# Performance work log

Hardware: AMD Instinct MI355X
Metric: run time of the kernel (lower is better)

Reference implementation:

```python
import jax, jax.numpy as jnp
import numpy as np

N_TOKEN = 32000
N_LAYER = 6
N_HEAD = 16
D_MODEL = 1024
D_HEAD = 64
D_INNER = 4096
QLEN = 512
MEM_LEN = 512
BSZ = 8
HD = N_HEAD * D_HEAD
SCALE = 1.0 / float(np.sqrt(D_HEAD))
NEG = -1e30


def _layer_norm(x, g, b, eps=1e-5):
    mu = jnp.mean(x, axis=-1, keepdims=True)
    var = jnp.var(x, axis=-1, keepdims=True)
    return (x - mu) * jax.lax.rsqrt(var + eps) * g + b


def _rel_shift(x):
    # x: [qlen, klen, bsz, n_head] -- TXL relative-position shift
    q, k, b, n = x.shape
    zp = jnp.zeros((q, 1, b, n), x.dtype)
    xp = jnp.concatenate([zp, x], axis=1).reshape(k + 1, q, b, n)
    return xp[1:].reshape(q, k, b, n)


def setup_inputs():
    key = jax.random.key(0)
    ks = jax.random.split(key, 12)
    s = 0.02
    rn = lambda k, *sh: jax.random.normal(k, sh, jnp.float32) * s
    z = lambda *sh: jnp.zeros(sh, jnp.float32)
    o = lambda *sh: jnp.ones(sh, jnp.float32)
    return {
        "data": jax.random.randint(ks[0], (QLEN, BSZ), 0, N_TOKEN),
        "target": jax.random.randint(ks[1], (QLEN, BSZ), 0, N_TOKEN),
        "memory": jax.random.normal(ks[2], (N_LAYER, MEM_LEN, BSZ, D_MODEL), jnp.float32),
        "emb_W": rn(ks[3], N_TOKEN, D_MODEL),  # tied input embedding / softmax head
        "r_w_bias": rn(ks[4], N_HEAD, D_HEAD),
        "r_r_bias": rn(ks[5], N_HEAD, D_HEAD),
        "Wq": rn(ks[6], N_LAYER, D_MODEL, HD),
        "Wkv": rn(ks[7], N_LAYER, D_MODEL, 2 * HD),
        "Wr": rn(ks[8], N_LAYER, D_MODEL, HD),
        "Wo": rn(ks[9], N_LAYER, HD, D_MODEL),
        "W1": rn(ks[10], N_LAYER, D_MODEL, D_INNER),
        "b1": z(N_LAYER, D_INNER),
        "W2": rn(ks[11], N_LAYER, D_INNER, D_MODEL),
        "b2": z(N_LAYER, D_MODEL),
        "ln1_g": o(N_LAYER, D_MODEL),
        "ln1_b": z(N_LAYER, D_MODEL),
        "ln2_g": o(N_LAYER, D_MODEL),
        "ln2_b": z(N_LAYER, D_MODEL),
    }


def _model(data, target, memory, emb_W, r_w_bias, r_r_bias, Wq, Wkv, Wr, Wo,
           W1, b1, W2, b2, ln1_g, ln1_b, ln2_g, ln2_b):
    qlen, bsz = data.shape
    mem = jax.lax.stop_gradient(memory)  # TXL detaches memories
    mlen = mem.shape[1]
    klen = mlen + qlen

    word_emb = emb_W[data]  # [q, b, d]

    # sinusoidal relative positions klen-1 .. 0
    pos_seq = jnp.arange(klen - 1, -1, -1, dtype=word_emb.dtype)
    inv_freq = 1.0 / (10000.0 ** (jnp.arange(0, D_MODEL, 2, dtype=word_emb.dtype) / D_MODEL))
    sin_inp = pos_seq[:, None] * inv_freq[None, :]
    pos = jnp.concatenate([jnp.sin(sin_inp), jnp.cos(sin_inp)], axis=-1)  # [klen, d]

    # causal mask with memory: query i can attend keys j <= i + mlen
    mask = jnp.arange(klen)[None, :] > (jnp.arange(qlen)[:, None] + mlen)  # [q, k]

    core = word_emb
    hids = [core]
    for i in range(N_LAYER):
        x_mem = jnp.concatenate([mem[i], core], axis=0)  # [klen, b, d]
        q = (core @ Wq[i]).reshape(qlen, bsz, N_HEAD, D_HEAD)
        kv = x_mem @ Wkv[i]
        k, v = jnp.split(kv, 2, axis=-1)
        k = k.reshape(klen, bsz, N_HEAD, D_HEAD)
        v = v.reshape(klen, bsz, N_HEAD, D_HEAD)
        r_k = (pos @ Wr[i]).reshape(klen, N_HEAD, D_HEAD)

        AC = jnp.einsum('ibnd,jbnd->ijbn', q + r_w_bias, k)
        BD = _rel_shift(jnp.einsum('ibnd,jnd->ijbn', q + r_r_bias, r_k))
        score = (AC + BD) * SCALE
        score = jnp.where(mask[:, :, None, None], NEG, score)
        prob = jax.nn.softmax(score, axis=1)
        vec = jnp.einsum('ijbn,jbnd->ibnd', prob, v).reshape(qlen, bsz, HD)
        attn_out = vec @ Wo[i]
        core = _layer_norm(core + attn_out, ln1_g[i], ln1_b[i])
        ff = jax.nn.relu(core @ W1[i] + b1[i]) @ W2[i] + b2[i]
        core = _layer_norm(core + ff, ln2_g[i], ln2_b[i])
        hids.append(core)

    # adaptive softmax with cutoffs=[] == full tied softmax
    logits = core @ emb_W.T  # [q, b, V]
    logp = jax.nn.log_softmax(logits, axis=-1)
    loss = -jnp.take_along_axis(logp, target[..., None], axis=-1)[..., 0]  # [q, b]

    new_mems = jnp.stack([
        jnp.concatenate([mem[i], hids[i]], axis=0)[-MEM_LEN:] for i in range(N_LAYER)
    ])
    new_mems = jax.lax.stop_gradient(new_mems)
    return loss, new_mems


def reference(data, target, memory, emb_W, r_w_bias, r_r_bias, Wq, Wkv, Wr, Wo,
              W1, b1, W2, b2, ln1_g, ln1_b, ln2_g, ln2_b):
    return _model(data, target, memory, emb_W, r_w_bias, r_r_bias, Wq, Wkv, Wr, Wo,
                  W1, b1, W2, b2, ln1_g, ln1_b, ln2_g, ln2_b)
```

## Files before the change

### kernel.cpp

```cpp
#include <hip/hip_runtime.h>
#include <hip/hip_bf16.h>
#include <math.h>

#define QLEN   512
#define MLEN   512
#define KLEN   1024
#define BSZ    8
#define NH     16
#define DH     64
#define DM     1024
#define DI     4096
#define NTOK   32000
#define NROW   4096
#define XROW   8192
#define VTILES 500

typedef __hip_bfloat16 bf16;
typedef __attribute__((ext_vector_type(8))) short bf16x8;
typedef __attribute__((ext_vector_type(4))) float f32x4;

__device__ __forceinline__ unsigned short f2b(float x) {
    union { float f; unsigned u; } a; a.f = x;
    unsigned r = a.u + 0x7fffu + ((a.u >> 16) & 1u);
    return (unsigned short)(r >> 16);
}
__device__ __forceinline__ float b2f(unsigned short h) {
    union { unsigned u; float f; } a; a.u = ((unsigned)h) << 16;
    return a.f;
}

__device__ __forceinline__ void gload_lds16(const void* g, void* l) {
    __builtin_amdgcn_global_load_lds(
        (const __attribute__((address_space(1))) unsigned int*)g,
        (__attribute__((address_space(3))) unsigned int*)l, 16, 0, 0);
}

__global__ __launch_bounds__(256) void posb_kernel(unsigned short* __restrict__ posb) {
    int j = blockIdx.x;
    int t = threadIdx.x;
    float p = (float)(1023 - j);
    #pragma unroll
    for (int u = 0; u < 4; u++) {
        int dcol = t + u * 256;
        int k = dcol & 511;
        float invf = expf(-((float)k) * (1.0f / 512.0f) * 9.210340371976184f);
        float a = p * invf;
        posb[j * DM + dcol] = f2b((dcol < 512) ? sinf(a) : cosf(a));
    }
}

__global__ __launch_bounds__(256) void gather_emb(const int* __restrict__ data,
                                                  const float* __restrict__ emb,
                                                  float* __restrict__ out,
                                                  unsigned short* __restrict__ outb) {
    int row = blockIdx.x;
    int t = threadIdx.x;
    int tok = data[row];
    float4 v = ((const float4*)(emb + (size_t)tok * DM))[t];
    ((float4*)(out + (size_t)row * DM))[t] = v;
    ushort4 o;
    o.x = f2b(v.x); o.y = f2b(v.y); o.z = f2b(v.z); o.w = f2b(v.w);
    ((ushort4*)(outb + (size_t)row * DM))[t] = o;
}

__global__ __launch_bounds__(256) void cast_bf16(const float* __restrict__ src,
                                                 unsigned short* __restrict__ dst, int n4) {
    int i = blockIdx.x * 256 + threadIdx.x;
    if (i < n4) {
        float4 v = ((const float4*)src)[i];
        ushort4 o;
        o.x = f2b(v.x); o.y = f2b(v.y); o.z = f2b(v.z); o.w = f2b(v.w);
        ((ushort4*)dst)[i] = o;
    }
}

__global__ __launch_bounds__(256) void castT_kernel(const float* __restrict__ src,
                                                    unsigned short* __restrict__ dst,
                                                    int K, int N) {
    __shared__ float T[32][33];
    int t = threadIdx.x;
    int k0 = blockIdx.y * 32, n0 = blockIdx.x * 32;
    int r = t >> 3, c4 = (t & 7) * 4;
    float4 v = *(const float4*)(src + (size_t)(k0 + r) * N + n0 + c4);
    T[r][c4 + 0] = v.x; T[r][c4 + 1] = v.y; T[r][c4 + 2] = v.z; T[r][c4 + 3] = v.w;
    __syncthreads();
    ushort4 o;
    o.x = f2b(T[c4 + 0][r]); o.y = f2b(T[c4 + 1][r]);
    o.z = f2b(T[c4 + 2][r]); o.w = f2b(T[c4 + 3][r]);
    *(ushort4*)(dst + (size_t)(n0 + r) * K + k0 + c4) = o;
}

template <bool BIAS, bool RELU, bool OUTBF16, int SPLITK = 1>
__global__ __launch_bounds__(256) void gemm_bt(const unsigned short* __restrict__ A,
                                               const unsigned short* __restrict__ B,
                                               const float* __restrict__ bias,
                                               void* __restrict__ Cout,
                                               int M, int N, int K) {
    __shared__ unsigned short As[128 * 32];
    __shared__ unsigned short Bs[128 * 32];
    int t = threadIdx.x;
    int wave = t >> 6, lane = t & 63;
    int bm = blockIdx.y * 128, bn = blockIdx.x * 128;
    int wm = (wave >> 1) * 64, wn = (wave & 1) * 64;
    int quad = lane >> 4, l16 = lane & 15;

    f32x4 acc[4][4] = {};

    int srow = wave * 32 + (lane >> 2);
    int scol = (lane & 3) * 8;
    const unsigned short* Ag = A + (size_t)(bm + srow) * K + scol;
    const unsigned short* Bg = B + (size_t)(bn + srow) * K + scol;
    unsigned short* Al0 = As + (wave * 32) * 32;
    unsigned short* Al1 = As + (wave * 32 + 16) * 32;
    unsigned short* Bl0 = Bs + (wave * 32) * 32;
    unsigned short* Bl1 = Bs + (wave * 32 + 16) * 32;

    int kchunk = K / SPLITK;
    int k0 = (SPLITK > 1) ? blockIdx.z * kchunk : 0;
    for (int kt = k0; kt < k0 + kchunk; kt += 32) {
        gload_lds16(Ag + kt, Al0);
        gload_lds16(Ag + kt + (size_t)16 * K, Al1);
        gload_lds16(Bg + kt, Bl0);
        gload_lds16(Bg + kt + (size_t)16 * K, Bl1);
        __syncthreads();
        bf16x8 af[4], bfr[4];
        #pragma unroll
        for (int mi = 0; mi < 4; mi++)
            af[mi] = *(const bf16x8*)&As[(wm + mi * 16 + l16) * 32 + quad * 8];
        #pragma unroll
        for (int ni = 0; ni < 4; ni++)
            bfr[ni] = *(const bf16x8*)&Bs[(wn + ni * 16 + l16) * 32 + quad * 8];
        #pragma unroll
        for (int mi = 0; mi < 4; mi++)
            #pragma unroll
            for (int ni = 0; ni < 4; ni++)
                acc[mi][ni] = __builtin_amdgcn_mfma_f32_16x16x32_bf16(
                    af[mi], bfr[ni], acc[mi][ni], 0, 0, 0);
        __syncthreads();
    }

    float* Cf = (float*)Cout + ((SPLITK > 1) ? (size_t)blockIdx.z * M * N : (size_t)0);
    #pragma unroll
    for (int mi = 0; mi < 4; mi++) {
        #pragma unroll
        for (int ni = 0; ni < 4; ni++) {
            int c = bn + wn + ni * 16 + l16;
            float bv = BIAS ? bias[c] : 0.0f;
            #pragma unroll
            for (int reg = 0; reg < 4; reg++) {
                int r = bm + wm + mi * 16 + quad * 4 + reg;
                float x = acc[mi][ni][reg];
                if (BIAS) x += bv;
                if (RELU) x = fmaxf(x, 0.0f);
                if (OUTBF16) ((unsigned short*)Cout)[(size_t)r * N + c] = f2b(x);
                else         Cf[(size_t)r * N + c] = x;
            }
        }
    }
}

__global__ __launch_bounds__(256) void kqv_gemm(const unsigned short* __restrict__ A,
                                                const unsigned short* __restrict__ B,
                                                const float* __restrict__ rwb,
                                                const float* __restrict__ rrb,
                                                unsigned short* __restrict__ qw,
                                                unsigned short* __restrict__ qr,
                                                unsigned short* __restrict__ Kh,
                                                unsigned short* __restrict__ Vth) {
    int cls = blockIdx.x >> 3;
    if (cls == 0 && blockIdx.y < 32) return;
    __shared__ unsigned short As[128 * 32];
    __shared__ unsigned short Bs[128 * 32];
    const int K = 1024;
    int t = threadIdx.x;
    int wave = t >> 6, lane = t & 63;
    int bm = blockIdx.y * 128, bn = blockIdx.x * 128;
    int wm = (wave >> 1) * 64, wn = (wave & 1) * 64;
    int quad = lane >> 4, l16 = lane & 15;

    f32x4 acc[4][4] = {};

    int srow = wave * 32 + (lane >> 2);
    int scol = (lane & 3) * 8;
    const unsigned short* Ag = A + (size_t)(bm + srow) * K + scol;
    const unsigned short* Bg = B + (size_t)(bn + srow) * K + scol;
    unsigned short* Al0 = As + (wave * 32) * 32;
    unsigned short* Al1 = As + (wave * 32 + 16) * 32;
    unsigned short* Bl0 = Bs + (wave * 32) * 32;
    unsigned short* Bl1 = Bs + (wave * 32 + 16) * 32;

    for (int kt = 0; kt < K; kt += 32) {
        gload_lds16(Ag + kt, Al0);
        gload_lds16(Ag + kt + (size_t)16 * K, Al1);
        gload_lds16(Bg + kt, Bl0);
        gload_lds16(Bg + kt + (size_t)16 * K, Bl1);
        __syncthreads();
        bf16x8 af[4], bfr[4];
        #pragma unroll
        for (int mi = 0; mi < 4; mi++)
            af[mi] = *(const bf16x8*)&As[(wm + mi * 16 + l16) * 32 + quad * 8];
        #pragma unroll
        for (int ni = 0; ni < 4; ni++)
            bfr[ni] = *(const bf16x8*)&Bs[(wn + ni * 16 + l16) * 32 + quad * 8];
        #pragma unroll
        for (int mi = 0; mi < 4; mi++)
            #pragma unroll
            for (int ni = 0; ni < 4; ni++)
                acc[mi][ni] = __builtin_amdgcn_mfma_f32_16x16x32_bf16(
                    af[mi], bfr[ni], acc[mi][ni], 0, 0, 0);
        __syncthreads();
    }

    if (cls == 0) {
        #pragma unroll
        for (int ni = 0; ni < 4; ni++) {
            int c = bn + wn + ni * 16 + l16;
            float wv = rwb[c], rv = rrb[c];
            #pragma unroll
            for (int mi = 0; mi < 4; mi++) {
                #pragma unroll
                for (int reg = 0; reg < 4; reg++) {
                    int r = bm + wm + mi * 16 + quad * 4 + reg;
                    int row = r - 4096;
                    int i = row >> 3;
                    float x = acc[mi][ni][reg];
                    qr[(size_t)row * DM + c] = f2b(x + rv);
                    qw[(size_t)row * DM + (c & ~63) + ((c & 63) ^ ((i & 7) << 3))] = f2b(x + wv);
                }
            }
        }
    } else if (cls == 1) {
        #pragma unroll
        for (int ni = 0; ni < 4; ni++) {
            int cc = bn + wn + ni * 16 + l16 - 1024;
            int d = cc & 63, hb = cc >> 6;
            #pragma unroll
            for (int mi = 0; mi < 4; mi++) {
                #pragma unroll
                for (int reg = 0; reg < 4; reg++) {
                    int r = bm + wm + mi * 16 + quad * 4 + reg;
                    int j = r >> 3, nb = hb * 8 + (r & 7);
                    Kh[(size_t)nb * 65536 + (size_t)j * 64 + (d ^ ((j & 7) << 3))] =
                        f2b(acc[mi][ni][reg]);
                }
            }
        }
    } else {
        #pragma unroll
        for (int ni = 0; ni < 4; ni++) {
            int cc = bn + wn + ni * 16 + l16 - 2048;
            int d = cc & 63, hb = cc >> 6;
            #pragma unroll
            for (int mi = 0; mi < 4; mi++) {
                #pragma unroll
                for (int reg = 0; reg < 4; reg++) {
                    int r = bm + wm + mi * 16 + quad * 4 + reg;
                    int j = r >> 3, nb = hb * 8 + (r & 7);
                    Vth[(size_t)nb * 65536 + (size_t)d * 1024
                        + (j & ~127) + ((j & 127) ^ ((d & 7) << 3))] =
                        f2b(acc[mi][ni][reg]);
                }
            }
        }
    }
}

__global__ __launch_bounds__(256) void lse_gemm_mfma(const unsigned short* __restrict__ A,
                                                     const unsigned short* __restrict__ B,
                                                     float* __restrict__ pmax,
                                                     float* __restrict__ psum) {
    __shared__ unsigned short As[128 * 32];
    __shared__ unsigned short Bs[128 * 32];
    int t = threadIdx.x;
    int wave = t >> 6, lane = t & 63;
    int bm = blockIdx.x * 128, bn = blockIdx.y * 128;
    int wm = (wave >> 1) * 64;
    int quad = lane >> 4, l16 = lane & 15;
    const int K = 1024;

    f32x4 acc[4][4] = {};

    int srow = wave * 32 + (lane >> 2);
    int scol = (lane & 3) * 8;
    const unsigned short* Ag = A + (size_t)(bm + srow) * K + scol;
    const unsigned short* Bg = B + (size_t)(bn + srow) * K + scol;
    unsigned short* Al0 = As + (wave * 32) * 32;
    unsigned short* Al1 = As + (wave * 32 + 16) * 32;
    unsigned short* Bl0 = Bs + (wave * 32) * 32;
    unsigned short* Bl1 = Bs + (wave * 32 + 16) * 32;
    int wn = (wave & 1) * 64;

    for (int kt = 0; kt < K; kt += 32) {
        gload_lds16(Ag + kt, Al0);
        gload_lds16(Ag + kt + (size_t)16 * K, Al1);
        gload_lds16(Bg + kt, Bl0);
        gload_lds16(Bg + kt + (size_t)16 * K, Bl1);
        __syncthreads();
        bf16x8 af[4], bfr[4];
        #pragma unroll
        for (int mi = 0; mi < 4; mi++)
            af[mi] = *(const bf16x8*)&As[(wm + mi * 16 + l16) * 32 + quad * 8];
        #pragma unroll
        for (int ni = 0; ni < 4; ni++)
            bfr[ni] = *(const bf16x8*)&Bs[(wn + ni * 16 + l16) * 32 + quad * 8];
        #pragma unroll
        for (int mi = 0; mi < 4; mi++)
            #pragma unroll
            for (int ni = 0; ni < 4; ni++)
                acc[mi][ni] = __builtin_amdgcn_mfma_f32_16x16x32_bf16(
                    af[mi], bfr[ni], acc[mi][ni], 0, 0, 0);
        __syncthreads();
    }

    int vt = blockIdx.y * 2 + (wave & 1);
    #pragma unroll
    for (int mi = 0; mi < 4; mi++) {
        #pragma unroll
        for (int reg = 0; reg < 4; reg++) {
            float m = -1e30f;
            #pragma unroll
            for (int ni = 0; ni < 4; ni++) m = fmaxf(m, acc[mi][ni][reg]);
            #pragma unroll
            for (int off = 1; off < 16; off <<= 1) m = fmaxf(m, __shfl_xor(m, off, 64));
            float s = 0.0f;
            #pragma unroll
            for (int ni = 0; ni < 4; ni++) s += __expf(acc[mi][ni][reg] - m);
            #pragma unroll
            for (int off = 1; off < 16; off <<= 1) s += __shfl_xor(s, off, 64);
            if (l16 == 0) {
                int r = bm + wm + mi * 16 + quad * 4 + reg;
                pmax[(size_t)r * VTILES + vt] = m;
                psum[(size_t)r * VTILES + vt] = s;
            }
        }
    }
}

__global__ __launch_bounds__(256) void bd_gemm(const unsigned short* __restrict__ A,
                                               const unsigned short* __restrict__ B,
                                               int ldb,
                                               unsigned short* __restrict__ Bt) {
    __shared__ unsigned short As[128 * 32];
    __shared__ unsigned short Bs[128 * 32];
    int t = threadIdx.x;
    int wave = t >> 6, lane = t & 63;
    int bm = blockIdx.y * 128, bn = blockIdx.x * 128, n = blockIdx.z;
    int wm = (wave >> 1) * 64, wn = (wave & 1) * 64;
    int quad = lane >> 4, l16 = lane & 15;
    f32x4 acc[4][4] = {};
    int srow = wave * 32 + (lane >> 2);
    int scol = (lane & 3) * 8;
    const unsigned short* Ag = A + (size_t)(bm + srow) * DM + n * 64 + scol;
    const unsigned short* Bg = B + (size_t)(bn + srow) * ldb + n * 64 + scol;
    unsigned short* Al0 = As + (wave * 32) * 32;
    unsigned short* Al1 = As + (wave * 32 + 16) * 32;
    unsigned short* Bl0 = Bs + (wave * 32) * 32;
    unsigned short* Bl1 = Bs + (wave * 32 + 16) * 32;

    #pragma unroll
    for (int kt = 0; kt < 64; kt += 32) {
        gload_lds16(Ag + kt, Al0);
        gload_lds16(Ag + kt + (size_t)16 * DM, Al1);
        gload_lds16(Bg + kt, Bl0);
        gload_lds16(Bg + kt + (size_t)16 * ldb, Bl1);
        __syncthreads();
        bf16x8 af[4], bfr[4];
        #pragma unroll
        for (int mi = 0; mi < 4; mi++)
            af[mi] = *(const bf16x8*)&As[(wm + mi * 16 + l16) * 32 + quad * 8];
        #pragma unroll
        for (int ni = 0; ni < 4; ni++)
            bfr[ni] = *(const bf16x8*)&Bs[(wn + ni * 16 + l16) * 32 + quad * 8];
        #pragma unroll
        for (int mi = 0; mi < 4; mi++)
            #pragma unroll
            for (int ni = 0; ni < 4; ni++)
                acc[mi][ni] = __builtin_amdgcn_mfma_f32_16x16x32_bf16(
                    af[mi], bfr[ni], acc[mi][ni], 0, 0, 0);
        __syncthreads();
    }

    #pragma unroll
    for (int mi = 0; mi < 4; mi++) {
        #pragma unroll
        for (int reg = 0; reg < 4; reg++) {
            int r = bm + wm + mi * 16 + quad * 4 + reg;
            int i = r >> 3;
            size_t rowbase = ((size_t)n * 4096 + r) * 1024;
            int sw = (i & 7) << 3;
            #pragma unroll
            for (int ni = 0; ni < 4; ni++) {
                int p = bn + wn + ni * 16 + l16;
                int j = p + i - 511;
                if ((unsigned)j < 1024u)
                    Bt[rowbase + (j & ~127) + ((j & 127) ^ sw)] = f2b(acc[mi][ni][reg]);
            }
        }
    }
}

__global__ __launch_bounds__(256) void flash_attn(const unsigned short* __restrict__ qw_b,
                                                  const unsigned short* __restrict__ Kh,
                                                  const unsigned short* __restrict__ Vth,
                                                  const unsigned short* __restrict__ Bt,
                                                  unsigned short* __restrict__ vecb) {
    int qb = blockIdx.x, b = blockIdx.y, n = blockIdx.z;
    int i0 = qb * 64, nb = n * 8 + b;
    int t = threadIdx.x, wave = t >> 6, lane = t & 63;
    int quad = lane >> 4, l16 = lane & 15;
    int wm = wave * 16;
    __shared__ unsigned short Qw_s[64 * 64];
    __shared__ unsigned short K_s[128 * 64];
    __shared__ unsigned short Vt_s[64 * 128];
    __shared__ unsigned short BD_s[64 * 128];

    {
        const unsigned short* g = qw_b
            + (size_t)((i0 + wave * 16 + (lane >> 3)) * 8 + b) * DM + n * 64 + (lane & 7) * 8;
        unsigned short* l = Qw_s + (wave * 16) * 64;
        gload_lds16(g, l);
        gload_lds16(g + (size_t)64 * DM, l + 8 * 64);
    }

    f32x4 o[4] = {};
    float m_run[4] = { -1e30f, -1e30f, -1e30f, -1e30f };
    float l_run[4] = {};

    int nt = ((i0 + 575) >> 7) + 1;
    for (int jt = 0; jt < nt; jt++) {
        int j0 = jt * 128;
        __syncthreads();
        {
            const unsigned short* g = Kh + (size_t)nb * 65536
                + (size_t)(j0 + wave * 32 + (lane >> 3)) * 64 + (lane & 7) * 8;
            unsigned short* l = K_s + (wave * 32) * 64;
            #pragma unroll
            for (int k = 0; k < 4; k++)
                gload_lds16(g + (size_t)k * 512, l + k * 512);
        }
        {
            const unsigned short* g = Vth + (size_t)nb * 65536
                + (size_t)(wave * 16 + (lane >> 4)) * 1024 + j0 + (lane & 15) * 8;
            unsigned short* l = Vt_s + (wave * 16) * 128;
            #pragma unroll
            for (int k = 0; k < 4; k++)
                gload_lds16(g + (size_t)k * 4096, l + k * 512);
        }
        {
            const unsigned short* g = Bt
                + ((size_t)n * 4096 + (size_t)(i0 + wave * 16 + (lane >> 4)) * 8 + b) * 1024
                + j0 + (lane & 15) * 8;
            unsigned short* l = BD_s + (wave * 16) * 128;
            #pragma unroll
            for (int k = 0; k < 4; k++)
                gload_lds16(g + (size_t)k * 32768, l + k * 512);
        }
        __syncthreads();

        int arow = wm + l16;
        int asw = (arow & 7) << 3;
        bf16x8 aq0 = *(const bf16x8*)&Qw_s[arow * 64 + ((quad * 8) ^ asw)];
        bf16x8 aq1 = *(const bf16x8*)&Qw_s[arow * 64 + ((32 + quad * 8) ^ asw)];
        f32x4 s[8];
        #pragma unroll
        for (int ni = 0; ni < 8; ni++) {
            int krow = ni * 16 + l16;
            int ksw = (krow & 7) << 3;
            bf16x8 b0 = *(const bf16x8*)&K_s[krow * 64 + ((quad * 8) ^ ksw)];
            bf16x8 b1 = *(const bf16x8*)&K_s[krow * 64 + ((32 + quad * 8) ^ ksw)];
            f32x4 z = {};
            z = __builtin_amdgcn_mfma_f32_16x16x32_bf16(aq0, b0, z, 0, 0, 0);
            s[ni] = __builtin_amdgcn_mfma_f32_16x16x32_bf16(aq1, b1, z, 0, 0, 0);
        }

        bool last = (jt == nt - 1);
        #pragma unroll
        for (int reg = 0; reg < 4; reg++) {
            int rl = quad * 4 + reg;
            int rsw = (rl & 7) << 3;
            #pragma unroll
            for (int ni = 0; ni < 8; ni++) {
                int c = ni * 16 + l16;
                float bd = b2f(BD_s[(wm + rl) * 128 + (c ^ rsw)]);
                float v = (s[ni][reg] + bd) * 0.125f;
                if (last && (j0 + c > i0 + wm + rl + 512)) v = -1e30f;
                s[ni][reg] = v;
            }
        }

        #pragma unroll
        for (int reg = 0; reg < 4; reg++) {
            float tm = s[0][reg];
            #pragma unroll
            for (int ni = 1; ni < 8; ni++) tm = fmaxf(tm, s[ni][reg]);
            #pragma unroll
            for (int off = 1; off < 16; off <<= 1) tm = fmaxf(tm, __shfl_xor(tm, off, 64));
            float mn = fmaxf(m_run[reg], tm);
            float alpha = __expf(m_run[reg] - mn);
            m_run[reg] = mn;
            float ts = 0.f;
            #pragma unroll
            for (int ni = 0; ni < 8; ni++) {
                float p = __expf(s[ni][reg] - mn);
                s[ni][reg] = p;
                ts += p;
            }
            #pragma unroll
            for (int off = 1; off < 16; off <<= 1) ts += __shfl_xor(ts, off, 64);
            l_run[reg] = l_run[reg] * alpha + ts;
            #pragma unroll
            for (int di = 0; di < 4; di++) o[di][reg] *= alpha;
        }

        #pragma unroll
        for (int reg = 0; reg < 4; reg++) {
            int rl = quad * 4 + reg;
            int rsw = (rl & 7) << 3;
            #pragma unroll
            for (int ni = 0; ni < 8; ni++) {
                int c = ni * 16 + l16;
                BD_s[(wm + rl) * 128 + (c ^ rsw)] = f2b(s[ni][reg]);
            }
        }

        #pragma unroll
        for (int kk = 0; kk < 4; kk++) {
            int prow = wm + l16;
            bf16x8 ap = *(const bf16x8*)&BD_s[prow * 128 + ((kk * 32 + quad * 8) ^ ((prow & 7) << 3))];
            #pragma unroll
            for (int di = 0; di < 4; di++) {
                int vr = di * 16 + l16;
                bf16x8 bv = *(const bf16x8*)&Vt_s[vr * 128 + ((kk * 32 + quad * 8) ^ ((vr & 7) << 3))];
                o[di] = __builtin_amdgcn_mfma_f32_16x16x32_bf16(ap, bv, o[di], 0, 0, 0);
            }
        }
    }

    #pragma unroll
    for (int reg = 0; reg < 4; reg++) {
        float inv = 1.0f / l_run[reg];
        int r = i0 + wm + quad * 4 + reg;
        #pragma unroll
        for (int di = 0; di < 4; di++) {
            vecb[(size_t)(r * 8 + b) * 1024 + n * 64 + di * 16 + l16] = f2b(o[di][reg] * inv);
        }
    }
}

template <int P, bool BIAS>
__global__ __launch_bounds__(256) void add_lnp(const float* __restrict__ x,
                                               const float* __restrict__ p,
                                               const float* __restrict__ bias,
                                               const float* __restrict__ g,
                                               const float* __restrict__ bb,
                                               float* __restrict__ outf,
                                               unsigned short* __restrict__ outb) {
    const size_t S = (size_t)NROW * DM;
    int row = blockIdx.x;
    int t = threadIdx.x;
    __shared__ float rs[256], rq[256];
    float v[4];
    float s = 0.f, sq = 0.f;
    #pragma unroll
    for (int u = 0; u < 4; u++) {
        int c = t + u * 256;
        size_t idx = (size_t)row * DM + c;
        float val = x[idx];
        if (BIAS) val += bias[c];
        #pragma unroll
        for (int k = 0; k < P; k++) val += p[(size_t)k * S + idx];
        v[u] = val;
        s += val;
        sq += val * val;
    }
    rs[t] = s;
    rq[t] = sq;
    __syncthreads();
    for (int off = 128; off > 0; off >>= 1) {
        if (t < off) { rs[t] += rs[t + off]; rq[t] += rq[t + off]; }
        __syncthreads();
    }
    float mu = rs[0] * (1.0f / 1024.0f);
    float var = rq[0] * (1.0f / 1024.0f) - mu * mu;
    float rstd = rsqrtf(var + 1e-5f);
    #pragma unroll
    for (int u = 0; u < 4; u++) {
        int c = t + u * 256;
        size_t idx = (size_t)row * DM + c;
        float o = (v[u] - mu) * rstd * g[c] + bb[c];
        outf[idx] = o;
        outb[idx] = f2b(o);
    }
}

__global__ __launch_bounds__(256) void tgt_logit_bf(const unsigned short* __restrict__ core,
                                                    const unsigned short* __restrict__ emb,
                                                    const int* __restrict__ target,
                                                    float* __restrict__ out) {
    int row = blockIdx.x;
    int t = threadIdx.x;
    __shared__ float red[256];
    int tok = target[row];
    const unsigned short* a = core + (size_t)row * DM;
    const unsigned short* e = emb + (size_t)tok * DM;
    float s = 0.f;
    #pragma unroll
    for (int u = 0; u < 4; u++) {
        int c = t + u * 256;
        s += b2f(a[c]) * b2f(e[c]);
    }
    red[t] = s;
    __syncthreads();
    for (int off = 128; off > 0; off >>= 1) {
        if (t < off) red[t] += red[t + off];
        __syncthreads();
    }
    if (t == 0) out[row] = red[0];
}

__global__ __launch_bounds__(256) void lse_reduce_kernel(const float* __restrict__ pmax,
                                                         const float* __restrict__ psum,
                                                         const float* __restrict__ ltgt,
                                                         float* __restrict__ loss) {
    int row = blockIdx.x;
    int t = threadIdx.x;
    __shared__ float red[256];
    float m = -1e30f;
    for (int u = t; u < VTILES; u += 256) m = fmaxf(m, pmax[(size_t)row * VTILES + u]);
    red[t] = m;
    __syncthreads();
    for (int off = 128; off > 0; off >>= 1) {
        if (t < off) red[t] = fmaxf(red[t], red[t + off]);
        __syncthreads();
    }
    float M = red[0];
    __syncthreads();
    float s = 0.f;
    for (int u = t; u < VTILES; u += 256)
        s += psum[(size_t)row * VTILES + u] * __expf(pmax[(size_t)row * VTILES + u] - M);
    red[t] = s;
    __syncthreads();
    for (int off = 128; off > 0; off >>= 1) {
        if (t < off) red[t] += red[t + off];
        __syncthreads();
    }
    if (t == 0) loss[row] = M + logf(red[0]) - ltgt[row];
}

extern "C" void kernel_launch(void* const* d_in, const int* in_sizes, int n_in,
                              void* d_out, int out_size, void* d_ws, size_t ws_size,
                              hipStream_t stream) {
    const int*   data   = (const int*)d_in[0];
    const int*   target = (const int*)d_in[1];
    const float* memory = (const float*)d_in[2];
    const float* embW   = (const float*)d_in[3];
    const float* rwb    = (const float*)d_in[4];
    const float* rrb    = (const float*)d_in[5];
    const float* Wq     = (const float*)d_in[6];
    const float* Wkv    = (const float*)d_in[7];
    const float* Wr     = (const float*)d_in[8];
    const float* Wo     = (const float*)d_in[9];
    const float* W1     = (const float*)d_in[10];
    const float* b1     = (const float*)d_in[11];
    const float* W2     = (const float*)d_in[12];
    const float* b2     = (const float*)d_in[13];
    const float* ln1g   = (const float*)d_in[14];
    const float* ln1b   = (const float*)d_in[15];
    const float* ln2g   = (const float*)d_in[16];
    const float* ln2b   = (const float*)d_in[17];

    float* out  = (float*)d_out;
    float* loss = out;
    float* hids = out + 4096;

    const size_t SZ_CORE = (size_t)NROW * DM;

    const size_t MB = 1024 * 1024;
    char* base = (char*)d_ws;
    unsigned short* posb   = (unsigned short*)(base);
    unsigned short* rkball = (unsigned short*)(base + 2 * MB);
    unsigned short* qw_b   = (unsigned short*)(base + 14 * MB);
    unsigned short* qr_b   = (unsigned short*)(base + 22 * MB);
    unsigned short* wTA    = (unsigned short*)(base + 30 * MB);
    unsigned short* vecb   = (unsigned short*)(base + 30 * MB);
    unsigned short* Kh     = (unsigned short*)(base + 38 * MB);
    unsigned short* Vth    = (unsigned short*)(base + 54 * MB);
    unsigned short* Bt     = (unsigned short*)(base + 70 * MB);
    unsigned short* memb   = (unsigned short*)(base + 70 * MB);
    unsigned short* cinb   = (unsigned short*)(base + 78 * MB);
    float*          cmid   = (float*)(base + 86 * MB);
    unsigned short* wrT    = (unsigned short*)(base + 86 * MB);
    unsigned short* wT     = (unsigned short*)(base + 14 * MB);
    unsigned short* cmidb  = (unsigned short*)(base + 22 * MB);
    float*          wop    = (float*)(base + 38 * MB);
    unsigned short* h1b    = (unsigned short*)(base + 102 * MB);
    float*          w2p    = (float*)(base + 134 * MB);
    float*          lnscr  = (float*)(base + 30 * MB);
    unsigned short* embWb  = (unsigned short*)(base + 86 * MB);
    float*          pmax   = (float*)(base + 152 * MB);
    float*          psum   = (float*)(base + 162 * MB);
    float*          ltgt   = (float*)(base + 172 * MB);
    unsigned short* corefnb = cinb;

    posb_kernel<<<KLEN, 256, 0, stream>>>(posb);
    gather_emb<<<NROW, 256, 0, stream>>>(data, embW, hids, cinb);

    for (int L = 0; L < 6; L++)
        castT_kernel<<<dim3(32, 32), 256, 0, stream>>>(
            Wr + (size_t)L * DM * DM, wrT + (size_t)L * DM * DM, DM, DM);
    gemm_bt<false, false, true><<<dim3(48, 8), 256, 0, stream>>>(
        posb, wrT, nullptr, rkball, KLEN, 6 * DM, DM);

    for (int L = 0; L < 6; L++) {
        const float* cin = hids + (size_t)L * SZ_CORE;
        float* coutf = (L < 5) ? (hids + (size_t)(L + 1) * SZ_CORE) : lnscr;

        cast_bf16<<<4096, 256, 0, stream>>>(memory + (size_t)L * SZ_CORE, memb, 1 << 20);

        castT_kernel<<<dim3(32, 32), 256, 0, stream>>>(Wq + (size_t)L * DM * DM, wTA, DM, DM);
        castT_kernel<<<dim3(64, 32), 256, 0, stream>>>(
            Wkv + (size_t)L * DM * 2 * DM, wTA + (size_t)DM * DM, DM, 2 * DM);
        kqv_gemm<<<dim3(24, 64), 256, 0, stream>>>(
            memb, wTA, rwb, rrb, qw_b, qr_b, Kh, Vth);

        bd_gemm<<<dim3(8, 32, 16), 256, 0, stream>>>(qr_b, rkball + (size_t)L * DM, 6 * DM, Bt);
        flash_attn<<<dim3(8, 8, 16), 256, 0, stream>>>(qw_b, Kh, Vth, Bt, vecb);

        castT_kernel<<<dim3(32, 32), 256, 0, stream>>>(Wo + (size_t)L * DM * DM, wT, DM, DM);
        gemm_bt<false, false, false, 2><<<dim3(8, 32, 2), 256, 0, stream>>>(
            vecb, wT, nullptr, wop, NROW, DM, DM);

        add_lnp<2, false><<<NROW, 256, 0, stream>>>(
            cin, wop, nullptr, ln1g + L * DM, ln1b + L * DM, cmid, cmidb);

        castT_kernel<<<dim3(128, 32), 256, 0, stream>>>(W1 + (size_t)L * DM * DI, wT, DM, DI);
        gemm_bt<true, true, true><<<dim3(32, 32), 256, 0, stream>>>(
            cmidb, wT, b1 + (size_t)L * DI, h1b, NROW, DI, DM);

        castT_kernel<<<dim3(32, 128), 256, 0, stream>>>(W2 + (size_t)L * DI * DM, wT, DI, DM);
        gemm_bt<false, false, false, 4><<<dim3(8, 32, 4), 256, 0, stream>>>(
            h1b, wT, nullptr, w2p, NROW, DM, DI);

        add_lnp<4, true><<<NROW, 256, 0, stream>>>(
            cmid, w2p, b2 + (size_t)L * DM, ln2g + L * DM, ln2b + L * DM, coutf, cinb);
    }

    cast_bf16<<<32768, 256, 0, stream>>>(embW, embWb, (NTOK * DM) / 4);
    tgt_logit_bf<<<NROW, 256, 0, stream>>>(corefnb, embWb, target, ltgt);
    lse_gemm_mfma<<<dim3(32, 250), 256, 0, stream>>>(corefnb, embWb, pmax, psum);
    lse_reduce_kernel<<<NROW, 256, 0, stream>>>(pmax, psum, ltgt, loss);
}
```

Baseline: 3.494 ms.

## Use K=64 swizzled LDS tiles in GEMMs, batch weight transposes, reduce split-K

Factors every MFMA GEMM main loop into a shared routine that stages 64-wide K tiles with an XOR swizzle, halving the barrier count and aiming to avoid LDS bank conflicts. Weight transpose-casts are merged into multi-matrix castT3 launches, cutting the number of kernel launches. The W2 GEMM drops from split-K 4 to 2, so fewer partial sums are written and reduced. The last layer's fp32 layer-norm output is now skipped. Doubling LDS per block may reduce occupancy, and buffer offsets were reshuffled, which risks aliasing between scratch regions.

```diff
diff --git a/kernel.cpp b/kernel.cpp
--- a/kernel.cpp
+++ b/kernel.cpp
@@ -35,6 +35,43 @@
         (__attribute__((address_space(3))) unsigned int*)l, 16, 0, 0);
 }
 
+__device__ __forceinline__ void kloop64(const unsigned short* __restrict__ Ag, int lda,
+                                        const unsigned short* __restrict__ Bg, int ldb,
+                                        unsigned short* As, unsigned short* Bs,
+                                        int wave, int lane, int wm, int wn,
+                                        int k0, int k1, f32x4 acc[4][4]) {
+    int quad = lane >> 4, l16 = lane & 15, asw = l16 & 7;
+    unsigned short* Al = As + (wave * 32) * 64;
+    unsigned short* Bl = Bs + (wave * 32) * 64;
+    for (int kt = k0; kt < k1; kt += 64) {
+        #pragma unroll
+        for (int k = 0; k < 4; k++) {
+            gload_lds16(Ag + kt + (size_t)(k * 8) * lda, Al + (k * 8) * 64);
+            gload_lds16(Bg + kt + (size_t)(k * 8) * ldb, Bl + (k * 8) * 64);
+        }
+        __syncthreads();
+        #pragma unroll
+        for (int kk = 0; kk < 2; kk++) {
+            bf16x8 af[4], bfr[4];
+            #pragma unroll
+            for (int mi = 0; mi < 4; mi++)
+                af[mi] = *(const bf16x8*)&As[(wm + mi * 16 + l16) * 64
+                                             + (((kk * 4 + quad) ^ asw) * 8)];
+            #pragma unroll
+            for (int ni = 0; ni < 4; ni++)
+                bfr[ni] = *(const bf16x8*)&Bs[(wn + ni * 16 + l16) * 64
+                                              + (((kk * 4 + quad) ^ asw) * 8)];
+            #pragma unroll
+            for (int mi = 0; mi < 4; mi++)
+                #pragma unroll
+                for (int ni = 0; ni < 4; ni++)
+                    acc[mi][ni] = __builtin_amdgcn_mfma_f32_16x16x32_bf16(
+                        af[mi], bfr[ni], acc[mi][ni], 0, 0, 0);
+        }
+        __syncthreads();
+    }
+}
+
 __global__ __launch_bounds__(256) void posb_kernel(unsigned short* __restrict__ posb) {
     int j = blockIdx.x;
     int t = threadIdx.x;
@@ -74,20 +111,30 @@
     }
 }
 
-__global__ __launch_bounds__(256) void castT_kernel(const float* __restrict__ src,
-                                                    unsigned short* __restrict__ dst,
-                                                    int K, int N) {
+__global__ __launch_bounds__(256) void castT3(const float* __restrict__ s0,
+                                              unsigned short* __restrict__ d0, int K0, int N0,
+                                              const float* __restrict__ s1,
+                                              unsigned short* __restrict__ d1, int K1, int N1,
+                                              const float* __restrict__ s2,
+                                              unsigned short* __restrict__ d2, int K2, int N2) {
+    int id = blockIdx.x;
+    const float* src; unsigned short* dst; int K, N;
+    int n0 = (N0 >> 5) * (K0 >> 5), n1 = (N1 >> 5) * (K1 >> 5);
+    if (id < n0)           { src = s0; dst = d0; K = K0; N = N0; }
+    else if (id < n0 + n1) { id -= n0; src = s1; dst = d1; K = K1; N = N1; }
+    else                   { id -= n0 + n1; src = s2; dst = d2; K = K2; N = N2; }
     __shared__ float T[32][33];
     int t = threadIdx.x;
-    int k0 = blockIdx.y * 32, n0 = blockIdx.x * 32;
+    int bx = id % (N >> 5), by = id / (N >> 5);
+    int k0 = by * 32, nc0 = bx * 32;
     int r = t >> 3, c4 = (t & 7) * 4;
-    float4 v = *(const float4*)(src + (size_t)(k0 + r) * N + n0 + c4);
+    float4 v = *(const float4*)(src + (size_t)(k0 + r) * N + nc0 + c4);
     T[r][c4 + 0] = v.x; T[r][c4 + 1] = v.y; T[r][c4 + 2] = v.z; T[r][c4 + 3] = v.w;
     __syncthreads();
     ushort4 o;
     o.x = f2b(T[c4 + 0][r]); o.y = f2b(T[c4 + 1][r]);
     o.z = f2b(T[c4 + 2][r]); o.w = f2b(T[c4 + 3][r]);
-    *(ushort4*)(dst + (size_t)(n0 + r) * K + k0 + c4) = o;
+    *(ushort4*)(dst + (size_t)(nc0 + r) * K + k0 + c4) = o;
 }
 
 template <bool BIAS, bool RELU, bool OUTBF16, int SPLITK = 1>
@@ -96,8 +143,8 @@
                                                const float* __restrict__ bias,
                                                void* __restrict__ Cout,
                                                int M, int N, int K) {
-    __shared__ unsigned short As[128 * 32];
-    __shared__ unsigned short Bs[128 * 32];
+    __shared__ unsigned short As[128 * 64];
+    __shared__ unsigned short Bs[128 * 64];
     int t = threadIdx.x;
     int wave = t >> 6, lane = t & 63;
     int bm = blockIdx.y * 128, bn = blockIdx.x * 128;
@@ -106,38 +153,14 @@
 
     f32x4 acc[4][4] = {};
 
-    int srow = wave * 32 + (lane >> 2);
-    int scol = (lane & 3) * 8;
+    int srow = wave * 32 + (lane >> 3);
+    int scol = ((lane & 7) ^ (srow & 7)) * 8;
     const unsigned short* Ag = A + (size_t)(bm + srow) * K + scol;
     const unsigned short* Bg = B + (size_t)(bn + srow) * K + scol;
-    unsigned short* Al0 = As + (wave * 32) * 32;
-    unsigned short* Al1 = As + (wave * 32 + 16) * 32;
-    unsigned short* Bl0 = Bs + (wave * 32) * 32;
-    unsigned short* Bl1 = Bs + (wave * 32 + 16) * 32;
 
     int kchunk = K / SPLITK;
     int k0 = (SPLITK > 1) ? blockIdx.z * kchunk : 0;
-    for (int kt = k0; kt < k0 + kchunk; kt += 32) {
-        gload_lds16(Ag + kt, Al0);
-        gload_lds16(Ag + kt + (size_t)16 * K, Al1);
-        gload_lds16(Bg + kt, Bl0);
-        gload_lds16(Bg + kt + (size_t)16 * K, Bl1);
-        __syncthreads();
-        bf16x8 af[4], bfr[4];
-        #pragma unroll
-        for (int mi = 0; mi < 4; mi++)
-            af[mi] = *(const bf16x8*)&As[(wm + mi * 16 + l16) * 32 + quad * 8];
-        #pragma unroll
-        for (int ni = 0; ni < 4; ni++)
-            bfr[ni] = *(const bf16x8*)&Bs[(wn + ni * 16 + l16) * 32 + quad * 8];
-        #pragma unroll
-        for (int mi = 0; mi < 4; mi++)
-            #pragma unroll
-            for (int ni = 0; ni < 4; ni++)
-                acc[mi][ni] = __builtin_amdgcn_mfma_f32_16x16x32_bf16(
-                    af[mi], bfr[ni], acc[mi][ni], 0, 0, 0);
-        __syncthreads();
-    }
+    kloop64(Ag, K, Bg, K, As, Bs, wave, lane, wm, wn, k0, k0 + kchunk, acc);
 
     float* Cf = (float*)Cout + ((SPLITK > 1) ? (size_t)blockIdx.z * M * N : (size_t)0);
     #pragma unroll
@@ -169,8 +192,8 @@
                                                 unsigned short* __restrict__ Vth) {
     int cls = blockIdx.x >> 3;
     if (cls == 0 && blockIdx.y < 32) return;
-    __shared__ unsigned short As[128 * 32];
-    __shared__ unsigned short Bs[128 * 32];
+    __shared__ unsigned short As[128 * 64];
+    __shared__ unsigned short Bs[128 * 64];
     const int K = 1024;
     int t = threadIdx.x;
     int wave = t >> 6, lane = t & 63;
@@ -180,36 +203,11 @@
 
     f32x4 acc[4][4] = {};
 
-    int srow = wave * 32 + (lane >> 2);
-    int scol = (lane & 3) * 8;
+    int srow = wave * 32 + (lane >> 3);
+    int scol = ((lane & 7) ^ (srow & 7)) * 8;
     const unsigned short* Ag = A + (size_t)(bm + srow) * K + scol;
     const unsigned short* Bg = B + (size_t)(bn + srow) * K + scol;
-    unsigned short* Al0 = As + (wave * 32) * 32;
-    unsigned short* Al1 = As + (wave * 32 + 16) * 32;
-    unsigned short* Bl0 = Bs + (wave * 32) * 32;
-    unsigned short* Bl1 = Bs + (wave * 32 + 16) * 32;
-
-    for (int kt = 0; kt < K; kt += 32) {
-        gload_lds16(Ag + kt, Al0);
-        gload_lds16(Ag + kt + (size_t)16 * K, Al1);
-        gload_lds16(Bg + kt, Bl0);
-        gload_lds16(Bg + kt + (size_t)16 * K, Bl1);
-        __syncthreads();
-        bf16x8 af[4], bfr[4];
-        #pragma unroll
-        for (int mi = 0; mi < 4; mi++)
-            af[mi] = *(const bf16x8*)&As[(wm + mi * 16 + l16) * 32 + quad * 8];
-        #pragma unroll
-        for (int ni = 0; ni < 4; ni++)
-            bfr[ni] = *(const bf16x8*)&Bs[(wn + ni * 16 + l16) * 32 + quad * 8];
-        #pragma unroll
-        for (int mi = 0; mi < 4; mi++)
-            #pragma unroll
-            for (int ni = 0; ni < 4; ni++)
-                acc[mi][ni] = __builtin_amdgcn_mfma_f32_16x16x32_bf16(
-                    af[mi], bfr[ni], acc[mi][ni], 0, 0, 0);
-        __syncthreads();
-    }
+    kloop64(Ag, K, Bg, K, As, Bs, wave, lane, wm, wn, 0, K, acc);
 
     if (cls == 0) {
         #pragma unroll
@@ -269,48 +267,22 @@
                                                      const unsigned short* __restrict__ B,
                                                      float* __restrict__ pmax,
                                                      float* __restrict__ psum) {
-    __shared__ unsigned short As[128 * 32];
-    __shared__ unsigned short Bs[128 * 32];
+    __shared__ unsigned short As[128 * 64];
+    __shared__ unsigned short Bs[128 * 64];
     int t = threadIdx.x;
     int wave = t >> 6, lane = t & 63;
     int bm = blockIdx.x * 128, bn = blockIdx.y * 128;
-    int wm = (wave >> 1) * 64;
+    int wm = (wave >> 1) * 64, wn = (wave & 1) * 64;
     int quad = lane >> 4, l16 = lane & 15;
     const int K = 1024;
 
     f32x4 acc[4][4] = {};
 
-    int srow = wave * 32 + (lane >> 2);
-    int scol = (lane & 3) * 8;
+    int srow = wave * 32 + (lane >> 3);
+    int scol = ((lane & 7) ^ (srow & 7)) * 8;
     const unsigned short* Ag = A + (size_t)(bm + srow) * K + scol;
     const unsigned short* Bg = B + (size_t)(bn + srow) * K + scol;
-    unsigned short* Al0 = As + (wave * 32) * 32;
-    unsigned short* Al1 = As + (wave * 32 + 16) * 32;
-    unsigned short* Bl0 = Bs + (wave * 32) * 32;
-    unsigned short* Bl1 = Bs + (wave * 32 + 16) * 32;
-    int wn = (wave & 1) * 64;
-
-    for (int kt = 0; kt < K; kt += 32) {
-        gload_lds16(Ag + kt, Al0);
-        gload_lds16(Ag + kt + (size_t)16 * K, Al1);
-        gload_lds16(Bg + kt, Bl0);
-        gload_lds16(Bg + kt + (size_t)16 * K, Bl1);
-        __syncthreads();
-        bf16x8 af[4], bfr[4];
-        #pragma unroll
-        for (int mi = 0; mi < 4; mi++)
-            af[mi] = *(const bf16x8*)&As[(wm + mi * 16 + l16) * 32 + quad * 8];
-        #pragma unroll
-        for (int ni = 0; ni < 4; ni++)
-            bfr[ni] = *(const bf16x8*)&Bs[(wn + ni * 16 + l16) * 32 + quad * 8];
-        #pragma unroll
-        for (int mi = 0; mi < 4; mi++)
-            #pragma unroll
-            for (int ni = 0; ni < 4; ni++)
-                acc[mi][ni] = __builtin_amdgcn_mfma_f32_16x16x32_bf16(
-                    af[mi], bfr[ni], acc[mi][ni], 0, 0, 0);
-        __syncthreads();
-    }
+    kloop64(Ag, K, Bg, K, As, Bs, wave, lane, wm, wn, 0, K, acc);
 
     int vt = blockIdx.y * 2 + (wave & 1);
     #pragma unroll
@@ -340,45 +312,19 @@
                                                const unsigned short* __restrict__ B,
                                                int ldb,
                                                unsigned short* __restrict__ Bt) {
-    __shared__ unsigned short As[128 * 32];
-    __shared__ unsigned short Bs[128 * 32];
+    __shared__ unsigned short As[128 * 64];
+    __shared__ unsigned short Bs[128 * 64];
     int t = threadIdx.x;
     int wave = t >> 6, lane = t & 63;
     int bm = blockIdx.y * 128, bn = blockIdx.x * 128, n = blockIdx.z;
     int wm = (wave >> 1) * 64, wn = (wave & 1) * 64;
     int quad = lane >> 4, l16 = lane & 15;
     f32x4 acc[4][4] = {};
-    int srow = wave * 32 + (lane >> 2);
-    int scol = (lane & 3) * 8;
+    int srow = wave * 32 + (lane >> 3);
+    int scol = ((lane & 7) ^ (srow & 7)) * 8;
     const unsigned short* Ag = A + (size_t)(bm + srow) * DM + n * 64 + scol;
     const unsigned short* Bg = B + (size_t)(bn + srow) * ldb + n * 64 + scol;
-    unsigned short* Al0 = As + (wave * 32) * 32;
-    unsigned short* Al1 = As + (wave * 32 + 16) * 32;
-    unsigned short* Bl0 = Bs + (wave * 32) * 32;
-    unsigned short* Bl1 = Bs + (wave * 32 + 16) * 32;
-
-    #pragma unroll
-    for (int kt = 0; kt < 64; kt += 32) {
-        gload_lds16(Ag + kt, Al0);
-        gload_lds16(Ag + kt + (size_t)16 * DM, Al1);
-        gload_lds16(Bg + kt, Bl0);
-        gload_lds16(Bg + kt + (size_t)16 * ldb, Bl1);
-        __syncthreads();
-        bf16x8 af[4], bfr[4];
-        #pragma unroll
-        for (int mi = 0; mi < 4; mi++)
-            af[mi] = *(const bf16x8*)&As[(wm + mi * 16 + l16) * 32 + quad * 8];
-        #pragma unroll
-        for (int ni = 0; ni < 4; ni++)
-            bfr[ni] = *(const bf16x8*)&Bs[(wn + ni * 16 + l16) * 32 + quad * 8];
-        #pragma unroll
-        for (int mi = 0; mi < 4; mi++)
-            #pragma unroll
-            for (int ni = 0; ni < 4; ni++)
-                acc[mi][ni] = __builtin_amdgcn_mfma_f32_16x16x32_bf16(
-                    af[mi], bfr[ni], acc[mi][ni], 0, 0, 0);
-        __syncthreads();
-    }
+    kloop64(Ag, DM, Bg, ldb, As, Bs, wave, lane, wm, wn, 0, 64, acc);
 
     #pragma unroll
     for (int mi = 0; mi < 4; mi++) {
@@ -588,7 +534,7 @@
         int c = t + u * 256;
         size_t idx = (size_t)row * DM + c;
         float o = (v[u] - mu) * rstd * g[c] + bb[c];
-        outf[idx] = o;
+        if (outf) outf[idx] = o;
         outb[idx] = f2b(o);
     }
 }
@@ -690,12 +636,13 @@
     unsigned short* cinb   = (unsigned short*)(base + 78 * MB);
     float*          cmid   = (float*)(base + 86 * MB);
     unsigned short* wrT    = (unsigned short*)(base + 86 * MB);
-    unsigned short* wT     = (unsigned short*)(base + 14 * MB);
-    unsigned short* cmidb  = (unsigned short*)(base + 22 * MB);
+    unsigned short* W1T    = (unsigned short*)(base + 14 * MB);
+    unsigned short* W2T    = (unsigned short*)(base + 22 * MB);
+    unsigned short* WoT    = (unsigned short*)(base + 134 * MB);
     float*          wop    = (float*)(base + 38 * MB);
     unsigned short* h1b    = (unsigned short*)(base + 102 * MB);
     float*          w2p    = (float*)(base + 134 * MB);
-    float*          lnscr  = (float*)(base + 30 * MB);
+    unsigned short* cmidb  = (unsigned short*)(base + 166 * MB);
     unsigned short* embWb  = (unsigned short*)(base + 86 * MB);
     float*          pmax   = (float*)(base + 152 * MB);
     float*          psum   = (float*)(base + 162 * MB);
@@ -705,43 +652,52 @@
     posb_kernel<<<KLEN, 256, 0, stream>>>(posb);
     gather_emb<<<NROW, 256, 0, stream>>>(data, embW, hids, cinb);
 
-    for (int L = 0; L < 6; L++)
-        castT_kernel<<<dim3(32, 32), 256, 0, stream>>>(
-            Wr + (size_t)L * DM * DM, wrT + (size_t)L * DM * DM, DM, DM);
+    castT3<<<3072, 256, 0, stream>>>(
+        Wr,                      wrT,                      DM, DM,
+        Wr + (size_t)1 * DM * DM, wrT + (size_t)1 * DM * DM, DM, DM,
+        Wr + (size_t)2 * DM * DM, wrT + (size_t)2 * DM * DM, DM, DM);
+    castT3<<<3072, 256, 0, stream>>>(
+        Wr + (size_t)3 * DM * DM, wrT + (size_t)3 * DM * DM, DM, DM,
+        Wr + (size_t)4 * DM * DM, wrT + (size_t)4 * DM * DM, DM, DM,
+        Wr + (size_t)5 * DM * DM, wrT + (size_t)5 * DM * DM, DM, DM);
     gemm_bt<false, false, true><<<dim3(48, 8), 256, 0, stream>>>(
         posb, wrT, nullptr, rkball, KLEN, 6 * DM, DM);
 
     for (int L = 0; L < 6; L++) {
         const float* cin = hids + (size_t)L * SZ_CORE;
-        float* coutf = (L < 5) ? (hids + (size_t)(L + 1) * SZ_CORE) : lnscr;
+        float* coutf = (L < 5) ? (hids + (size_t)(L + 1) * SZ_CORE) : nullptr;
 
         cast_bf16<<<4096, 256, 0, stream>>>(memory + (size_t)L * SZ_CORE, memb, 1 << 20);
 
-        castT_kernel<<<dim3(32, 32), 256, 0, stream>>>(Wq + (size_t)L * DM * DM, wTA, DM, DM);
-        castT_kernel<<<dim3(64, 32), 256, 0, stream>>>(
-            Wkv + (size_t)L * DM * 2 * DM, wTA + (size_t)DM * DM, DM, 2 * DM);
+        castT3<<<3072, 256, 0, stream>>>(
+            Wq + (size_t)L * DM * DM,      wTA,                    DM, DM,
+            Wkv + (size_t)L * DM * 2 * DM, wTA + (size_t)DM * DM,  DM, 2 * DM,
+            Wq, wTA, 32, 32);
+
         kqv_gemm<<<dim3(24, 64), 256, 0, stream>>>(
             memb, wTA, rwb, rrb, qw_b, qr_b, Kh, Vth);
 
         bd_gemm<<<dim3(8, 32, 16), 256, 0, stream>>>(qr_b, rkball + (size_t)L * DM, 6 * DM, Bt);
         flash_attn<<<dim3(8, 8, 16), 256, 0, stream>>>(qw_b, Kh, Vth, Bt, vecb);
 
-        castT_kernel<<<dim3(32, 32), 256, 0, stream>>>(Wo + (size_t)L * DM * DM, wT, DM, DM);
+        castT3<<<9216, 256, 0, stream>>>(
+            Wo + (size_t)L * DM * DM, WoT, DM, DM,
+            W1 + (size_t)L * DM * DI, W1T, DM, DI,
+            W2 + (size_t)L * DI * DM, W2T, DI, DM);
+
         gemm_bt<false, false, false, 2><<<dim3(8, 32, 2), 256, 0, stream>>>(
-            vecb, wT, nullptr, wop, NROW, DM, DM);
+            vecb, WoT, nullptr, wop, NROW, DM, DM);
 
         add_lnp<2, false><<<NROW, 256, 0, stream>>>(
             cin, wop, nullptr, ln1g + L * DM, ln1b + L * DM, cmid, cmidb);
 
-        castT_kernel<<<dim3(128, 32), 256, 0, stream>>>(W1 + (size_t)L * DM * DI, wT, DM, DI);
         gemm_bt<true, true, true><<<dim3(32, 32), 256, 0, stream>>>(
-            cmidb, wT, b1 + (size_t)L * DI, h1b, NROW, DI, DM);
-
-        castT_kernel<<<dim3(32, 128), 256, 0, stream>>>(W2 + (size_t)L * DI * DM, wT, DI, DM);
-        gemm_bt<false, false, false, 4><<<dim3(8, 32, 4), 256, 0, stream>>>(
-            h1b, wT, nullptr, w2p, NROW, DM, DI);
-
-        add_lnp<4, true><<<NROW, 256, 0, stream>>>(
+            cmidb, W1T, b1 + (size_t)L * DI, h1b, NROW, DI, DM);
+
+        gemm_bt<false, false, false, 2><<<dim3(8, 32, 2), 256, 0, stream>>>(
+            h1b, W2T, nullptr, w2p, NROW, DM, DI);
+
+        add_lnp<2, true><<<NROW, 256, 0, stream>>>(
             cmid, w2p, b2 + (size_t)L * DM, ln2g + L * DM, ln2b + L * DM, coutf, cinb);
     }
 
```

Result: faster. 3.192 ms (median of 2 runs) (-8.6%).
